# Optimization experiments

Measured on AMD Instinct MI355X. Metric: run time of the kernel, lower is better.

The kernel has to match this reference:

```python
import jax, jax.numpy as jnp
import numpy as np

HIDDEN = 1024
HEADS = 16
HEAD_DIM = HIDDEN // HEADS
SPARSITY_RATIO = 0.5


def setup_inputs() -> dict:
    key = jax.random.key(0)
    ks = jax.random.split(key, 6)
    B, S = 2, 2048
    # Xavier-uniform for square Linear weights: limit = sqrt(6/(fan_in+fan_out))
    lim = float(np.sqrt(6.0 / (HIDDEN + HIDDEN)))
    x = jax.random.normal(ks[0], (B, S, HIDDEN), dtype=jnp.float32)
    Wq = jax.random.uniform(ks[1], (HIDDEN, HIDDEN), minval=-lim, maxval=lim, dtype=jnp.float32)
    Wk = jax.random.uniform(ks[2], (HIDDEN, HIDDEN), minval=-lim, maxval=lim, dtype=jnp.float32)
    Wv = jax.random.uniform(ks[3], (HIDDEN, HIDDEN), minval=-lim, maxval=lim, dtype=jnp.float32)
    Wo = jax.random.uniform(ks[4], (HIDDEN, HIDDEN), minval=-lim, maxval=lim, dtype=jnp.float32)
    bo = jnp.zeros((HIDDEN,), dtype=jnp.float32)
    adaptive_threshold = jnp.asarray(0.1, dtype=jnp.float32)
    return {"x": x, "Wq": Wq, "Wk": Wk, "Wv": Wv, "Wo": Wo, "bo": bo,
            "adaptive_threshold": adaptive_threshold}


def reference(x, Wq, Wk, Wv, Wo, bo, adaptive_threshold):
    B, S, _ = x.shape
    H, D = HEADS, HEAD_DIM
    # projections (torch Linear: y = x @ W.T), split heads -> [B, H, S, D]
    q = (x @ Wq.T).reshape(B, S, H, D).transpose(0, 2, 1, 3)
    k = (x @ Wk.T).reshape(B, S, H, D).transpose(0, 2, 1, 3)
    v = (x @ Wv.T).reshape(B, S, H, D).transpose(0, 2, 1, 3)
    scores = jnp.einsum('bhqd,bhkd->bhqk', q, k) / jnp.sqrt(jnp.asarray(D, x.dtype))
    # adaptive top-k sparsity: keep top k entries per query row
    k_keep = max(1, int(S * (1.0 - SPARSITY_RATIO)))
    topv = jax.lax.top_k(scores, k_keep)[0]          # [B,H,S,k]
    kth = topv[..., -1:]                              # k-th largest per row
    thr = jnp.clip(adaptive_threshold, 0.0, 1.0)
    keep = (scores >= kth) & (scores >= thr)
    neg_inf = jnp.asarray(-jnp.inf, scores.dtype)
    masked = jnp.where(keep, scores, neg_inf)
    attn = jax.nn.softmax(masked, axis=-1)            # dropout is no-op in eval
    out = jnp.einsum('bhqk,bhkd->bhqd', attn, v)      # [B,H,S,D]
    out = out.transpose(0, 2, 1, 3).reshape(B, S, H * D)
    return out @ Wo.T + bo
```

## Files before the change

### kernel.cpp

```cpp
#include <hip/hip_runtime.h>
#include <hip/hip_bf16.h>
#include <cstdint>
#include <cstddef>

#define HIDDEN 1024
#define HEADS  16
#define HDIM   64
#define BATCH  2
#define SEQ    2048
#define MTOT   (BATCH*SEQ)
#define KSEL   1024
#define QT     16

typedef __attribute__((ext_vector_type(8))) short bf16x8;
typedef __attribute__((ext_vector_type(4))) float f32x4;

__device__ __forceinline__ unsigned short f2bf_rne(float f) {
    unsigned u = __float_as_uint(f);
    u += 0x7fffu + ((u >> 16) & 1u);
    return (unsigned short)(u >> 16);
}
__device__ __forceinline__ float bf2f(unsigned short h) {
    return __uint_as_float(((unsigned)h) << 16);
}
__device__ __forceinline__ int score_bucket(float v) {
    int b = (int)floorf(__fmaf_rn(v, 32.0f, 256.0f));
    return min(511, max(0, b));
}
__device__ __forceinline__ void gl2lds16(const unsigned short* g, unsigned short* l) {
    __builtin_amdgcn_global_load_lds(
        (const __attribute__((address_space(1))) unsigned int*)g,
        (__attribute__((address_space(3))) unsigned int*)l, 16, 0, 0);
}

__global__ __launch_bounds__(256) void split_bf(
    const float* __restrict__ src, unsigned short* __restrict__ hi,
    unsigned short* __restrict__ lo, int n4)
{
    int i = blockIdx.x * 256 + threadIdx.x;
    if (i >= n4) return;
    float4 v = ((const float4*)src)[i];
    unsigned short h0 = f2bf_rne(v.x), h1 = f2bf_rne(v.y);
    unsigned short h2 = f2bf_rne(v.z), h3 = f2bf_rne(v.w);
    uint2 hv, lv;
    hv.x = (unsigned)h0 | ((unsigned)h1 << 16);
    hv.y = (unsigned)h2 | ((unsigned)h3 << 16);
    lv.x = (unsigned)f2bf_rne(v.x - bf2f(h0)) | ((unsigned)f2bf_rne(v.y - bf2f(h1)) << 16);
    lv.y = (unsigned)f2bf_rne(v.z - bf2f(h2)) | ((unsigned)f2bf_rne(v.w - bf2f(h3)) << 16);
    *(uint2*)(hi + (size_t)i * 4) = hv;
    *(uint2*)(lo + (size_t)i * 4) = lv;
}

__device__ __forceinline__ void gemm_mainloop(
    const unsigned short* __restrict__ Ah, const unsigned short* __restrict__ Al,
    const unsigned short* __restrict__ Bh, const unsigned short* __restrict__ Bl,
    int n0, int m0, unsigned short* lds, f32x4 acc[4][4])
{
    const int t = threadIdx.x;
    const int lane = t & 63;
    const int wid = t >> 6;
    const int wn = wid & 1, wm = wid >> 1;
    const int quad = lane >> 4, n16 = lane & 15;

    unsigned short* lAh = lds;
    unsigned short* lAl = lds + 4096;
    unsigned short* lBh = lds + 8192;
    unsigned short* lBl = lds + 12288;

    int rowp[2], cp[2];
#pragma unroll
    for (int p = 0; p < 2; ++p) {
        int cidx = p * 256 + t;
        rowp[p] = cidx >> 2;
        cp[p]   = (cidx & 3) ^ ((rowp[p] >> 1) & 3);
    }
    const int wbase = (t >> 6) * 64;

    int offA[4], offB[4];
#pragma unroll
    for (int i = 0; i < 4; ++i) {
        int ra = wn * 64 + i * 16 + n16;
        offA[i] = ra * 32 + (quad ^ ((ra >> 1) & 3)) * 8;
        int rb = wm * 64 + i * 16 + n16;
        offB[i] = rb * 32 + (quad ^ ((rb >> 1) & 3)) * 8;
    }

    for (int k0 = 0; k0 < HIDDEN; k0 += 32) {
        __syncthreads();
#pragma unroll
        for (int p = 0; p < 2; ++p) {
            const size_t aoff = (size_t)(n0 + rowp[p]) * HIDDEN + k0 + cp[p] * 8;
            const size_t boff = (size_t)(m0 + rowp[p]) * HIDDEN + k0 + cp[p] * 8;
            const int ldst = (p * 256 + wbase) * 8;
            gl2lds16(Ah + aoff, lAh + ldst);
            gl2lds16(Al + aoff, lAl + ldst);
            gl2lds16(Bh + boff, lBh + ldst);
            gl2lds16(Bl + boff, lBl + ldst);
        }
        __syncthreads();

        bf16x8 fah[4], fal[4], fbh[4], fbl[4];
#pragma unroll
        for (int i = 0; i < 4; ++i) {
            fah[i] = *(const bf16x8*)(lAh + offA[i]);
            fal[i] = *(const bf16x8*)(lAl + offA[i]);
            fbh[i] = *(const bf16x8*)(lBh + offB[i]);
            fbl[i] = *(const bf16x8*)(lBl + offB[i]);
        }
#pragma unroll
        for (int i = 0; i < 4; ++i)
#pragma unroll
            for (int j = 0; j < 4; ++j) {
                acc[i][j] = __builtin_amdgcn_mfma_f32_16x16x32_bf16(fah[i], fbh[j], acc[i][j], 0, 0, 0);
                acc[i][j] = __builtin_amdgcn_mfma_f32_16x16x32_bf16(fah[i], fbl[j], acc[i][j], 0, 0, 0);
                acc[i][j] = __builtin_amdgcn_mfma_f32_16x16x32_bf16(fal[i], fbh[j], acc[i][j], 0, 0, 0);
            }
    }
}

__global__ __launch_bounds__(256) void qkv_gemm(
    const unsigned short* __restrict__ xh, const unsigned short* __restrict__ xl,
    const unsigned short* __restrict__ Wsp,
    unsigned short* __restrict__ Qh, unsigned short* __restrict__ Ql,
    unsigned short* __restrict__ Kh, unsigned short* __restrict__ Kl,
    unsigned short* __restrict__ Vt)
{
    __shared__ __align__(16) unsigned short lds[16384];
    const int z = blockIdx.z;
    const unsigned short* Wh = Wsp + (size_t)z * 2097152;
    const unsigned short* Wl = Wh + 1048576;
    const int m0 = blockIdx.x * 128, n0 = blockIdx.y * 128;

    f32x4 acc[4][4];
#pragma unroll
    for (int i = 0; i < 4; ++i)
#pragma unroll
        for (int j = 0; j < 4; ++j) acc[i][j] = (f32x4){0.f, 0.f, 0.f, 0.f};

    gemm_mainloop(Wh, Wl, xh, xl, n0, m0, lds, acc);

    const int t = threadIdx.x;
    const int lane = t & 63, wid = t >> 6;
    const int wn = wid & 1, wm = wid >> 1;
    const int quad = lane >> 4, n16 = lane & 15;
    const float scale = (z == 0) ? 0.125f : 1.0f;

    if (z < 2) {
        unsigned short* oh = z ? Kh : Qh;
        unsigned short* ol = z ? Kl : Ql;
#pragma unroll
        for (int i = 0; i < 4; ++i)
#pragma unroll
            for (int j = 0; j < 4; ++j) {
                int m  = m0 + wm * 64 + j * 16 + n16;
                int nn = n0 + wn * 64 + i * 16 + quad * 4;
                int bb = m >> 11, ss = m & (SEQ - 1);
                int hh = nn >> 6, dd = nn & 63;
                size_t base = ((size_t)(bb * HEADS + hh) * SEQ + ss) * HDIM + dd;
                unsigned short h[4], l[4];
#pragma unroll
                for (int r = 0; r < 4; ++r) {
                    float v = acc[i][j][r] * scale;
                    h[r] = f2bf_rne(v);
                    l[r] = f2bf_rne(v - bf2f(h[r]));
                }
                uint2 hv, lv;
                hv.x = (unsigned)h[0] | ((unsigned)h[1] << 16);
                hv.y = (unsigned)h[2] | ((unsigned)h[3] << 16);
                lv.x = (unsigned)l[0] | ((unsigned)l[1] << 16);
                lv.y = (unsigned)l[2] | ((unsigned)l[3] << 16);
                *(uint2*)(oh + base) = hv;
                *(uint2*)(ol + base) = lv;
            }
    } else {
#pragma unroll
        for (int i = 0; i < 4; ++i)
#pragma unroll
            for (int j = 0; j < 4; ++j) {
                int m  = m0 + wm * 64 + j * 16 + n16;
                int bb = m >> 11, ss = m & (SEQ - 1);
#pragma unroll
                for (int r = 0; r < 4; ++r) {
                    int nn = n0 + wn * 64 + i * 16 + quad * 4 + r;
                    int hh = nn >> 6, dd = nn & 63;
                    Vt[((size_t)(bb * HEADS + hh) * HDIM + dd) * SEQ + ss] =
                        f2bf_rne(acc[i][j][r]);
                }
            }
    }
}

__global__ __launch_bounds__(256) void out_gemm(
    const unsigned short* __restrict__ Oh, const unsigned short* __restrict__ Ol,
    const unsigned short* __restrict__ Woh, const unsigned short* __restrict__ Wol,
    const float* __restrict__ bias, float* __restrict__ out)
{
    __shared__ __align__(16) unsigned short lds[16384];
    const int m0 = blockIdx.x * 128, n0 = blockIdx.y * 128;

    f32x4 acc[4][4];
#pragma unroll
    for (int i = 0; i < 4; ++i)
#pragma unroll
        for (int j = 0; j < 4; ++j) acc[i][j] = (f32x4){0.f, 0.f, 0.f, 0.f};

    gemm_mainloop(Woh, Wol, Oh, Ol, n0, m0, lds, acc);

    const int t = threadIdx.x;
    const int lane = t & 63, wid = t >> 6;
    const int wn = wid & 1, wm = wid >> 1;
    const int quad = lane >> 4, n16 = lane & 15;
#pragma unroll
    for (int i = 0; i < 4; ++i)
#pragma unroll
        for (int j = 0; j < 4; ++j) {
            int m  = m0 + wm * 64 + j * 16 + n16;
            int nn = n0 + wn * 64 + i * 16 + quad * 4;
            float4 v;
            v.x = acc[i][j][0] + bias[nn + 0];
            v.y = acc[i][j][1] + bias[nn + 1];
            v.z = acc[i][j][2] + bias[nn + 2];
            v.w = acc[i][j][3] + bias[nn + 3];
            *(float4*)&out[(size_t)m * HIDDEN + nn] = v;
        }
}

__global__ __launch_bounds__(256, 2) void attn_mfma(
    const unsigned short* __restrict__ Qh, const unsigned short* __restrict__ Ql,
    const unsigned short* __restrict__ Kh, const unsigned short* __restrict__ Kl,
    const unsigned short* __restrict__ Vt, const float* __restrict__ thrp,
    unsigned short* __restrict__ Oh, unsigned short* __restrict__ Ol)
{
    __shared__ __align__(16) unsigned short Ks[16384];
    __shared__ __align__(16) unsigned char U[33792];
    __shared__ __align__(16) float cand[16][64];
    __shared__ __align__(16) float Olds[16][64];
    __shared__ float smax[4][16], ssum[4][16];
    __shared__ unsigned csum[16][16];
    __shared__ float gmax[16], gsum[16], cutv[16];
    __shared__ int bcut[16], resid[16];
    __shared__ unsigned ccnt[16];

    const int t = threadIdx.x;
    const int lane = t & 63, wid = t >> 6;
    const int quad = lane >> 4, n16 = lane & 15;
    const int bh = (blockIdx.x & 7) + 8 * (int)(blockIdx.x >> 10);
    const int q0 = ((blockIdx.x >> 3) & 127) * QT;
    const int row0 = quad * 4;

    unsigned* hist = (unsigned*)U;
    unsigned short* Pww = (unsigned short*)(U + wid * 1024);

    const float thv = fminf(fmaxf(thrp[0], 0.f), 1.f);

    for (int j = t; j < 16*513; j += 256) hist[j] = 0u;
    for (int j = t; j < 16*64; j += 256) ((float*)Olds)[j] = 0.f;
    if (t < 16) ccnt[t] = 0u;

    const size_t qoff = ((size_t)bh*SEQ + q0 + n16)*HDIM + quad*8;
    bf16x8 aqh0 = *(const bf16x8*)(Qh + qoff);
    bf16x8 aqh1 = *(const bf16x8*)(Qh + qoff + 32);
    bf16x8 aql0 = *(const bf16x8*)(Ql + qoff);
    bf16x8 aql1 = *(const bf16x8*)(Ql + qoff + 32);

    const unsigned short* khb = Kh + (size_t)bh*SEQ*HDIM;
    const unsigned short* klb = Kl + (size_t)bh*SEQ*HDIM;
    unsigned short* KsH = Ks;
    unsigned short* KsL = Ks + 8192;

    f32x4 sc[32];
#pragma unroll
    for (int c = 0; c < 16; ++c) {
        __syncthreads();
#pragma unroll
        for (int s = 0; s < 4; ++s) {
            int idx = s*256 + t;
            int row = idx >> 3, pc = idx & 7;
            int schunk = pc ^ (row & 7);
            const size_t goff = (size_t)(c*128 + row)*HDIM + schunk*8;
            gl2lds16(khb + goff, KsH + idx*8);
            gl2lds16(klb + goff, KsL + idx*8);
        }
        __syncthreads();
#pragma unroll
        for (int i = 0; i < 2; ++i) {
            int r = wid*32 + i*16 + n16;
            int p0 = (quad ^ (r & 7)) * 8;
            int p1 = ((quad + 4) ^ (r & 7)) * 8;
            bf16x8 kb0 = *(const bf16x8*)(KsH + r*64 + p0);
            bf16x8 kb1 = *(const bf16x8*)(KsH + r*64 + p1);
            bf16x8 kl0 = *(const bf16x8*)(KsL + r*64 + p0);
            bf16x8 kl1 = *(const bf16x8*)(KsL + r*64 + p1);
            f32x4 a = {0.f, 0.f, 0.f, 0.f};
            a = __builtin_amdgcn_mfma_f32_16x16x32_bf16(aqh0, kb0, a, 0, 0, 0);
            a = __builtin_amdgcn_mfma_f32_16x16x32_bf16(aqh1, kb1, a, 0, 0, 0);
            a = __builtin_amdgcn_mfma_f32_16x16x32_bf16(aqh0, kl0, a, 0, 0, 0);
            a = __builtin_amdgcn_mfma_f32_16x16x32_bf16(aqh1, kl1, a, 0, 0, 0);
            a = __builtin_amdgcn_mfma_f32_16x16x32_bf16(aql0, kb0, a, 0, 0, 0);
            a = __builtin_amdgcn_mfma_f32_16x16x32_bf16(aql1, kb1, a, 0, 0, 0);
            sc[c*2 + i] = a;
        }
    }

    float rmax[4];
#pragma unroll
    for (int r = 0; r < 4; ++r) {
        float v = sc[0][r];
#pragma unroll
        for (int tt = 1; tt < 32; ++tt) v = fmaxf(v, sc[tt][r]);
#pragma unroll
        for (int m = 1; m < 16; m <<= 1) v = fmaxf(v, __shfl_xor(v, m));
        rmax[r] = v;
    }
    if (n16 == 0) {
#pragma unroll
        for (int r = 0; r < 4; ++r) smax[wid][row0 + r] = rmax[r];
    }
    __syncthreads();
    if (t < 16) gmax[t] = fmaxf(fmaxf(smax[0][t], smax[1][t]),
                                fmaxf(smax[2][t], smax[3][t]));

#pragma unroll
    for (int tt = 0; tt < 32; ++tt)
#pragma unroll
        for (int r = 0; r < 4; ++r)
            atomicAdd(&hist[(row0 + r)*513 + score_bucket(sc[tt][r])], 1u);
    __syncthreads();

    {
        int row = t >> 4, slot = t & 15;
        int btop = 512 - slot*32;
        unsigned s = 0;
        for (int b = btop - 32; b < btop; ++b) s += hist[row*513 + b];
        csum[row][slot] = s;
    }
    __syncthreads();

    if (t < 16) {
        unsigned cs[16];
#pragma unroll
        for (int j = 0; j < 16; ++j) cs[j] = csum[t][j];
        unsigned cum = 0; int jc = -1;
#pragma unroll
        for (int j = 0; j < 16; ++j) {
            bool here = (jc < 0) && (cum + cs[j] >= (unsigned)KSEL);
            if (here) jc = j;
            if (jc < 0) cum += cs[j];
        }
        int btop = 512 - jc*32;
        unsigned hb[32];
#pragma unroll 4
        for (int i = 0; i < 32; ++i) hb[i] = hist[t*513 + btop - 1 - i];
        unsigned c2 = cum; int bsel = btop - 32; int rres = 1; bool found = false;
#pragma unroll
        for (int i = 0; i < 32; ++i) {
            bool here = !found && (c2 + hb[i] >= (unsigned)KSEL);
            if (here) { bsel = btop - 1 - i; rres = KSEL - (int)c2; found = true; }
            if (!found) c2 += hb[i];
        }
        bcut[t] = bsel; resid[t] = rres;
        cutv[t] = ((float)bsel - 256.0f) * 0.03125f;
    }
    __syncthreads();

    {
        int bc[4];
#pragma unroll
        for (int r = 0; r < 4; ++r) bc[r] = bcut[row0 + r];
#pragma unroll
        for (int tt = 0; tt < 32; ++tt)
#pragma unroll
            for (int r = 0; r < 4; ++r) {
                float v = sc[tt][r];
                if (score_bucket(v) == bc[r]) {
                    unsigned idx = atomicAdd(&ccnt[row0 + r], 1u);
                    if (idx < 64u) cand[row0 + r][idx] = v;
                }
            }
    }
    __syncthreads();

    {
        int row = t >> 4, slot = t & 15;
        int n = min((int)ccnt[row], 64);
        int r = resid[row];
        for (int i = slot; i < n; i += 16) {
            float c = cand[row][i];
            int gt = 0, ge = 0;
            for (int j = 0; j < n; ++j) {
                float x = cand[row][j];
                gt += (x > c); ge += (x >= c);
            }
            if (gt < r && ge >= r) cutv[row] = c;
        }
    }
    __syncthreads();

    float mrow[4], crow[4], l4[4];
#pragma unroll
    for (int r = 0; r < 4; ++r) {
        mrow[r] = gmax[row0 + r];
        crow[r] = fmaxf(cutv[row0 + r], thv);
        l4[r] = 0.f;
    }
    f32x4 oacc[4];
#pragma unroll
    for (int dt = 0; dt < 4; ++dt) oacc[dt] = (f32x4){0.f, 0.f, 0.f, 0.f};
    const unsigned short* vtb = Vt + (size_t)bh*HDIM*SEQ;
    unsigned short* Vs = Ks;

#pragma unroll
    for (int c = 0; c < 16; ++c) {
        __syncthreads();
#pragma unroll
        for (int s = 0; s < 4; ++s) {
            int idx = s*256 + t;
            int row = idx >> 4, pc = idx & 15;
            int schunk = pc ^ (row & 15);
            gl2lds16(vtb + (size_t)row*SEQ + c*128 + schunk*8, Vs + idx*8);
        }
#pragma unroll
        for (int i = 0; i < 2; ++i)
#pragma unroll
            for (int r = 0; r < 4; ++r) {
                float v = sc[c*2 + i][r];
                float p = (v >= crow[r]) ? __expf(v - mrow[r]) : 0.f;
                l4[r] += p;
                Pww[(row0 + r)*32 + i*16 + n16] = f2bf_rne(p);
            }
        __syncthreads();
        bf16x8 af = *(const bf16x8*)(Pww + n16*32 + quad*8);
#pragma unroll
        for (int dt = 0; dt < 4; ++dt) {
            int vrow = dt*16 + n16;
            int pos = ((wid*4 + quad) ^ (vrow & 15)) * 8;
            bf16x8 bf = *(const bf16x8*)(Vs + vrow*128 + pos);
            oacc[dt] = __builtin_amdgcn_mfma_f32_16x16x32_bf16(af, bf, oacc[dt], 0, 0, 0);
        }
    }

#pragma unroll
    for (int r = 0; r < 4; ++r) {
#pragma unroll
        for (int m = 1; m < 16; m <<= 1) l4[r] += __shfl_xor(l4[r], m);
    }
    if (n16 == 0) {
#pragma unroll
        for (int r = 0; r < 4; ++r) ssum[wid][row0 + r] = l4[r];
    }
#pragma unroll
    for (int dt = 0; dt < 4; ++dt)
#pragma unroll
        for (int r = 0; r < 4; ++r)
            atomicAdd(&Olds[row0 + r][dt*16 + n16], oacc[dt][r]);
    __syncthreads();
    if (t < 16) gsum[t] = ssum[0][t] + ssum[1][t] + ssum[2][t] + ssum[3][t];
    __syncthreads();
    {
        int row = t >> 4, d4 = (t & 15) * 4;
        float inv = 1.0f / gsum[row];
        float o0 = Olds[row][d4+0] * inv, o1 = Olds[row][d4+1] * inv;
        float o2 = Olds[row][d4+2] * inv, o3 = Olds[row][d4+3] * inv;
        unsigned short h0 = f2bf_rne(o0), h1 = f2bf_rne(o1);
        unsigned short h2 = f2bf_rne(o2), h3 = f2bf_rne(o3);
        uint2 hv, lv;
        hv.x = (unsigned)h0 | ((unsigned)h1 << 16);
        hv.y = (unsigned)h2 | ((unsigned)h3 << 16);
        lv.x = (unsigned)f2bf_rne(o0 - bf2f(h0)) | ((unsigned)f2bf_rne(o1 - bf2f(h1)) << 16);
        lv.y = (unsigned)f2bf_rne(o2 - bf2f(h2)) | ((unsigned)f2bf_rne(o3 - bf2f(h3)) << 16);
        const int bb = bh >> 4, hh = bh & 15;
        size_t base = ((size_t)(bb*SEQ + q0 + row))*HIDDEN + hh*HDIM + d4;
        *(uint2*)(Oh + base) = hv;
        *(uint2*)(Ol + base) = lv;
    }
}

extern "C" void kernel_launch(void* const* d_in, const int* in_sizes, int n_in,
                              void* d_out, int out_size, void* d_ws, size_t ws_size,
                              hipStream_t stream)
{
    (void)in_sizes; (void)n_in; (void)out_size; (void)ws_size;
    const float* x  = (const float*)d_in[0];
    const float* Wq = (const float*)d_in[1];
    const float* Wk = (const float*)d_in[2];
    const float* Wv = (const float*)d_in[3];
    const float* Wo = (const float*)d_in[4];
    const float* bo = (const float*)d_in[5];
    const float* at = (const float*)d_in[6];
    float* out = (float*)d_out;

    char* ws = (char*)d_ws;
    const size_t MB = 1048576;
    unsigned short* xh  = (unsigned short*)(ws);
    unsigned short* xl  = (unsigned short*)(ws + 8*MB);
    unsigned short* Wsp = (unsigned short*)(ws + 16*MB);
    unsigned short* Qh  = (unsigned short*)(ws + 32*MB);
    unsigned short* Ql  = (unsigned short*)(ws + 40*MB);
    unsigned short* Kh  = (unsigned short*)(ws + 48*MB);
    unsigned short* Kl  = (unsigned short*)(ws + 56*MB);
    unsigned short* Vt  = (unsigned short*)d_out;

    split_bf<<<MTOT*HIDDEN/4/256, 256, 0, stream>>>(x,  xh, xl, MTOT*HIDDEN/4);
    split_bf<<<HIDDEN*HIDDEN/4/256, 256, 0, stream>>>(Wq, Wsp + 0u*1048576u, Wsp + 1u*1048576u, HIDDEN*HIDDEN/4);
    split_bf<<<HIDDEN*HIDDEN/4/256, 256, 0, stream>>>(Wk, Wsp + 2u*1048576u, Wsp + 3u*1048576u, HIDDEN*HIDDEN/4);
    split_bf<<<HIDDEN*HIDDEN/4/256, 256, 0, stream>>>(Wv, Wsp + 4u*1048576u, Wsp + 5u*1048576u, HIDDEN*HIDDEN/4);
    split_bf<<<HIDDEN*HIDDEN/4/256, 256, 0, stream>>>(Wo, Wsp + 6u*1048576u, Wsp + 7u*1048576u, HIDDEN*HIDDEN/4);

    qkv_gemm<<<dim3(MTOT/128, HIDDEN/128, 3), 256, 0, stream>>>(xh, xl, Wsp, Qh, Ql, Kh, Kl, Vt);
    attn_mfma<<<BATCH*HEADS*(SEQ/QT), 256, 0, stream>>>(Qh, Ql, Kh, Kl, Vt, at, xh, xl);
    out_gemm<<<dim3(MTOT/128, HIDDEN/128, 1), 256, 0, stream>>>(xh, xl, Wsp + 6u*1048576u, Wsp + 7u*1048576u, bo, out);
}
```

Measured before the change: 765.6 us.

## Recompute QK scores per pass instead of holding them in registers

Result: slower. 837.9 us (+9.5%).

```diff
diff --git a/kernel.cpp b/kernel.cpp
--- a/kernel.cpp
+++ b/kernel.cpp
@@ -249,7 +249,6 @@
     const int row0 = quad * 4;
 
     unsigned* hist = (unsigned*)U;
-    unsigned short* Pww = (unsigned short*)(U + wid * 1024);
 
     const float thv = fminf(fmaxf(thrp[0], 0.f), 1.f);
 
@@ -268,16 +267,22 @@
     unsigned short* KsH = Ks;
     unsigned short* KsL = Ks + 8192;
 
-    f32x4 sc[32];
-#pragma unroll
+    int krow[4], kpc[4];
+#pragma unroll
+    for (int s = 0; s < 4; ++s) {
+        int idx = s*256 + t;
+        krow[s] = idx >> 3;
+        kpc[s]  = (idx & 3 | (idx & 7)) & 7;
+        kpc[s]  = (idx & 7) ^ (krow[s] & 7);
+    }
+
+    float rmax[4] = {-1e30f, -1e30f, -1e30f, -1e30f};
     for (int c = 0; c < 16; ++c) {
         __syncthreads();
 #pragma unroll
         for (int s = 0; s < 4; ++s) {
-            int idx = s*256 + t;
-            int row = idx >> 3, pc = idx & 7;
-            int schunk = pc ^ (row & 7);
-            const size_t goff = (size_t)(c*128 + row)*HDIM + schunk*8;
+            const size_t goff = (size_t)(c*128 + krow[s])*HDIM + kpc[s]*8;
+            const int idx = s*256 + t;
             gl2lds16(khb + goff, KsH + idx*8);
             gl2lds16(klb + goff, KsL + idx*8);
         }
@@ -298,19 +303,17 @@
             a = __builtin_amdgcn_mfma_f32_16x16x32_bf16(aqh1, kl1, a, 0, 0, 0);
             a = __builtin_amdgcn_mfma_f32_16x16x32_bf16(aql0, kb0, a, 0, 0, 0);
             a = __builtin_amdgcn_mfma_f32_16x16x32_bf16(aql1, kb1, a, 0, 0, 0);
-            sc[c*2 + i] = a;
-        }
-    }
-
-    float rmax[4];
+#pragma unroll
+            for (int r4 = 0; r4 < 4; ++r4) {
+                rmax[r4] = fmaxf(rmax[r4], a[r4]);
+                atomicAdd(&hist[(row0 + r4)*513 + score_bucket(a[r4])], 1u);
+            }
+        }
+    }
 #pragma unroll
     for (int r = 0; r < 4; ++r) {
-        float v = sc[0][r];
-#pragma unroll
-        for (int tt = 1; tt < 32; ++tt) v = fmaxf(v, sc[tt][r]);
-#pragma unroll
-        for (int m = 1; m < 16; m <<= 1) v = fmaxf(v, __shfl_xor(v, m));
-        rmax[r] = v;
+#pragma unroll
+        for (int m = 1; m < 16; m <<= 1) rmax[r] = fmaxf(rmax[r], __shfl_xor(rmax[r], m));
     }
     if (n16 == 0) {
 #pragma unroll
@@ -319,13 +322,6 @@
     __syncthreads();
     if (t < 16) gmax[t] = fmaxf(fmaxf(smax[0][t], smax[1][t]),
                                 fmaxf(smax[2][t], smax[3][t]));
-
-#pragma unroll
-    for (int tt = 0; tt < 32; ++tt)
-#pragma unroll
-        for (int r = 0; r < 4; ++r)
-            atomicAdd(&hist[(row0 + r)*513 + score_bucket(sc[tt][r])], 1u);
-    __syncthreads();
 
     {
         int row = t >> 4, slot = t & 15;
@@ -367,16 +363,41 @@
         int bc[4];
 #pragma unroll
         for (int r = 0; r < 4; ++r) bc[r] = bcut[row0 + r];
-#pragma unroll
-        for (int tt = 0; tt < 32; ++tt)
-#pragma unroll
-            for (int r = 0; r < 4; ++r) {
-                float v = sc[tt][r];
-                if (score_bucket(v) == bc[r]) {
-                    unsigned idx = atomicAdd(&ccnt[row0 + r], 1u);
-                    if (idx < 64u) cand[row0 + r][idx] = v;
+        for (int c = 0; c < 16; ++c) {
+            __syncthreads();
+#pragma unroll
+            for (int s = 0; s < 4; ++s) {
+                const size_t goff = (size_t)(c*128 + krow[s])*HDIM + kpc[s]*8;
+                const int idx = s*256 + t;
+                gl2lds16(khb + goff, KsH + idx*8);
+                gl2lds16(klb + goff, KsL + idx*8);
+            }
+            __syncthreads();
+#pragma unroll
+            for (int i = 0; i < 2; ++i) {
+                int r = wid*32 + i*16 + n16;
+                int p0 = (quad ^ (r & 7)) * 8;
+                int p1 = ((quad + 4) ^ (r & 7)) * 8;
+                bf16x8 kb0 = *(const bf16x8*)(KsH + r*64 + p0);
+                bf16x8 kb1 = *(const bf16x8*)(KsH + r*64 + p1);
+                bf16x8 kl0 = *(const bf16x8*)(KsL + r*64 + p0);
+                bf16x8 kl1 = *(const bf16x8*)(KsL + r*64 + p1);
+                f32x4 a = {0.f, 0.f, 0.f, 0.f};
+                a = __builtin_amdgcn_mfma_f32_16x16x32_bf16(aqh0, kb0, a, 0, 0, 0);
+                a = __builtin_amdgcn_mfma_f32_16x16x32_bf16(aqh1, kb1, a, 0, 0, 0);
+                a = __builtin_amdgcn_mfma_f32_16x16x32_bf16(aqh0, kl0, a, 0, 0, 0);
+                a = __builtin_amdgcn_mfma_f32_16x16x32_bf16(aqh1, kl1, a, 0, 0, 0);
+                a = __builtin_amdgcn_mfma_f32_16x16x32_bf16(aql0, kb0, a, 0, 0, 0);
+                a = __builtin_amdgcn_mfma_f32_16x16x32_bf16(aql1, kb1, a, 0, 0, 0);
+#pragma unroll
+                for (int r4 = 0; r4 < 4; ++r4) {
+                    if (score_bucket(a[r4]) == bc[r4]) {
+                        unsigned idx2 = atomicAdd(&ccnt[row0 + r4], 1u);
+                        if (idx2 < 64u) cand[row0 + r4][idx2] = a[r4];
+                    }
                 }
             }
+        }
     }
     __syncthreads();
 
@@ -407,28 +428,46 @@
 #pragma unroll
     for (int dt = 0; dt < 4; ++dt) oacc[dt] = (f32x4){0.f, 0.f, 0.f, 0.f};
     const unsigned short* vtb = Vt + (size_t)bh*HDIM*SEQ;
-    unsigned short* Vs = Ks;
-
-#pragma unroll
+    unsigned short* Vs  = (unsigned short*)U;
+    unsigned short* Pww = (unsigned short*)(U + 16384) + wid * 512;
+
     for (int c = 0; c < 16; ++c) {
         __syncthreads();
 #pragma unroll
         for (int s = 0; s < 4; ++s) {
-            int idx = s*256 + t;
-            int row = idx >> 4, pc = idx & 15;
-            int schunk = pc ^ (row & 15);
-            gl2lds16(vtb + (size_t)row*SEQ + c*128 + schunk*8, Vs + idx*8);
-        }
-#pragma unroll
-        for (int i = 0; i < 2; ++i)
-#pragma unroll
-            for (int r = 0; r < 4; ++r) {
-                float v = sc[c*2 + i][r];
-                float p = (v >= crow[r]) ? __expf(v - mrow[r]) : 0.f;
-                l4[r] += p;
-                Pww[(row0 + r)*32 + i*16 + n16] = f2bf_rne(p);
-            }
+            const size_t goff = (size_t)(c*128 + krow[s])*HDIM + kpc[s]*8;
+            const int idx = s*256 + t;
+            gl2lds16(khb + goff, KsH + idx*8);
+            gl2lds16(klb + goff, KsL + idx*8);
+            int vrow = idx >> 4, vpc = idx & 15;
+            int vsch = vpc ^ (vrow & 15);
+            gl2lds16(vtb + (size_t)vrow*SEQ + c*128 + vsch*8, Vs + idx*8);
+        }
         __syncthreads();
+#pragma unroll
+        for (int i = 0; i < 2; ++i) {
+            int r = wid*32 + i*16 + n16;
+            int p0 = (quad ^ (r & 7)) * 8;
+            int p1 = ((quad + 4) ^ (r & 7)) * 8;
+            bf16x8 kb0 = *(const bf16x8*)(KsH + r*64 + p0);
+            bf16x8 kb1 = *(const bf16x8*)(KsH + r*64 + p1);
+            bf16x8 kl0 = *(const bf16x8*)(KsL + r*64 + p0);
+            bf16x8 kl1 = *(const bf16x8*)(KsL + r*64 + p1);
+            f32x4 a = {0.f, 0.f, 0.f, 0.f};
+            a = __builtin_amdgcn_mfma_f32_16x16x32_bf16(aqh0, kb0, a, 0, 0, 0);
+            a = __builtin_amdgcn_mfma_f32_16x16x32_bf16(aqh1, kb1, a, 0, 0, 0);
+            a = __builtin_amdgcn_mfma_f32_16x16x32_bf16(aqh0, kl0, a, 0, 0, 0);
+            a = __builtin_amdgcn_mfma_f32_16x16x32_bf16(aqh1, kl1, a, 0, 0, 0);
+            a = __builtin_amdgcn_mfma_f32_16x16x32_bf16(aql0, kb0, a, 0, 0, 0);
+            a = __builtin_amdgcn_mfma_f32_16x16x32_bf16(aql1, kb1, a, 0, 0, 0);
+#pragma unroll
+            for (int r4 = 0; r4 < 4; ++r4) {
+                float v = a[r4];
+                float p = (v >= crow[r4]) ? __expf(v - mrow[r4]) : 0.f;
+                l4[r4] += p;
+                Pww[(row0 + r4)*32 + i*16 + n16] = f2bf_rne(p);
+            }
+        }
         bf16x8 af = *(const bf16x8*)(Pww + n16*32 + quad*8);
 #pragma unroll
         for (int dt = 0; dt < 4; ++dt) {
```
